# Performance work log

Hardware: AMD Instinct MI355X
Metric: run time of the kernel (lower is better)

Reference implementation:

```python
import jax, jax.numpy as jnp
import numpy as np

B, S, DM = 4, 2048, 1024
H, D, R = 16, 64, 8

def setup_inputs() -> dict:
    key = jax.random.key(0)
    ks = jax.random.split(key, 32)
    def rn(k, shape, scale=0.02):
        return jax.random.normal(k, shape, dtype=jnp.float32) * scale
    inp = {
        'queries': jax.random.normal(ks[0], (B, S, DM), dtype=jnp.float32),
        'keys':    jax.random.normal(ks[1], (B, S, DM), dtype=jnp.float32),
        'values':  jax.random.normal(ks[2], (B, S, DM), dtype=jnp.float32),
        # base projections, stored [in, out]
        'Wq_w': rn(ks[3], (DM, H * D)), 'Wq_b': jnp.zeros((H * D,), jnp.float32),
        'Wk_w': rn(ks[4], (DM, H * D)), 'Wk_b': jnp.zeros((H * D,), jnp.float32),
        'Wv_w': rn(ks[5], (DM, H * D)), 'Wv_b': jnp.zeros((H * D,), jnp.float32),
        # LoRA adapters (A: in->rank, B: rank->out), Linear layers so both have biases
        'Aq_w': rn(ks[6], (DM, R)), 'Aq_b': jnp.zeros((R,), jnp.float32),
        'Bq_w': rn(ks[7], (R, H * D)), 'Bq_b': jnp.zeros((H * D,), jnp.float32),
        'Ak_w': rn(ks[8], (DM, R)), 'Ak_b': jnp.zeros((R,), jnp.float32),
        'Bk_w': rn(ks[9], (R, H * D)), 'Bk_b': jnp.zeros((H * D,), jnp.float32),
        'Av_w': rn(ks[10], (DM, R)), 'Av_b': jnp.zeros((R,), jnp.float32),
        'Bv_w': rn(ks[11], (R, H * D)), 'Bv_b': jnp.zeros((H * D,), jnp.float32),
        # output merge
        'Wo_w': rn(ks[12], (H * D, DM)), 'Wo_b': jnp.zeros((DM,), jnp.float32),
    }
    return inp


def _attn(queries, keys, values, Wq_w, Wq_b, Wk_w, Wk_b, Wv_w, Wv_b,
          Aq_w, Aq_b, Bq_w, Bq_b, Ak_w, Ak_b, Bk_w, Bk_b, Av_w, Av_b, Bv_w, Bv_b,
          Wo_w, Wo_b):
    b, s, _ = queries.shape
    # QKV projections fused with LoRA low-rank additions
    q = queries @ Wq_w + Wq_b + ((queries @ Aq_w + Aq_b) @ Bq_w + Bq_b)
    k = keys    @ Wk_w + Wk_b + ((keys    @ Ak_w + Ak_b) @ Bk_w + Bk_b)
    # NOTE: source applies the V LoRA adapter to `keys` (self.Av(keys)) - replicated
    v = values  @ Wv_w + Wv_b + ((keys    @ Av_w + Av_b) @ Bv_w + Bv_b)
    q = q.reshape(b, s, H, D).transpose(0, 2, 1, 3)  # [B,H,S,D]
    k = k.reshape(b, s, H, D).transpose(0, 2, 1, 3)
    v = v.reshape(b, s, H, D).transpose(0, 2, 1, 3)
    att = jnp.einsum('bhqd,bhkd->bhqk', q, k)        # [B,H,Sq,Sk]
    causal = jnp.tril(jnp.ones((s, s), dtype=bool))
    att = jnp.where(causal, att, -jnp.inf)
    # NOTE: source softmaxes over dim=2 (query axis) and scales AFTER softmax
    att = jax.nn.softmax(att, axis=2) / jnp.sqrt(jnp.asarray(D, att.dtype))
    out = jnp.einsum('bhqk,bhkd->bhqd', att, v)      # [B,H,S,D]
    out = out.transpose(0, 2, 1, 3).reshape(b, s, H * D)
    return out @ Wo_w + Wo_b


def reference(queries, keys, values, Wq_w, Wq_b, Wk_w, Wk_b, Wv_w, Wv_b,
              Aq_w, Aq_b, Bq_w, Bq_b, Ak_w, Ak_b, Bk_w, Bk_b, Av_w, Av_b, Bv_w, Bv_b,
              Wo_w, Wo_b):
    return _attn(queries, keys, values, Wq_w, Wq_b, Wk_w, Wk_b, Wv_w, Wv_b,
                 Aq_w, Aq_b, Bq_w, Bq_b, Ak_w, Ak_b, Bk_w, Bk_b, Av_w, Av_b, Bv_w, Bv_b,
                 Wo_w, Wo_b)
```

## Files before the change

### kernel.cpp

```cpp
#include <hip/hip_runtime.h>
#include <math.h>
#include <stdint.h>

typedef __bf16 bf16;
typedef __bf16 bf16x8 __attribute__((ext_vector_type(8)));
typedef __bf16 bf16x4 __attribute__((ext_vector_type(4)));
typedef float  floatx4 __attribute__((ext_vector_type(4)));

#define MFMA16(a, b, c) __builtin_amdgcn_mfma_f32_16x16x32_bf16(a, b, c, 0, 0, 0)
#define EXP2(x) __builtin_amdgcn_exp2f(x)

static constexpr int S  = 2048;
static constexpr int DM = 1024;
static constexpr int Dh = 64;
static constexpr size_t QBSZ = (size_t)64 * 2048 * 64;
#define NEGBIG (-1e30f)
#define LOG2E  1.44269504088896340736f

__device__ __forceinline__ void gload16(const void* g, void* l) {
  __builtin_amdgcn_global_load_lds(
      (const __attribute__((address_space(1))) void*)(uintptr_t)g,
      (__attribute__((address_space(3))) void*)(uintptr_t)l,
      16, 0, 0);
}

__device__ __forceinline__ int swz(int row, int g) {
  return row * 64 + ((g ^ (row & 7)) << 3);
}

__global__ __launch_bounds__(256) void prep_convert(
    const float* __restrict__ q, const float* __restrict__ k,
    const float* __restrict__ v, bf16* __restrict__ X)
{
  int s = blockIdx.x;
  int c = threadIdx.x * 4;
  size_t src = (size_t)s * DM + c;
  float4 qv = *(const float4*)(q + src);
  float4 vv = *(const float4*)(v + src);
  float4 kv = *(const float4*)(k + src);
  size_t dst = (size_t)s * (3 * DM);
  bf16x4 t;
  t[0] = (bf16)qv.x; t[1] = (bf16)qv.y; t[2] = (bf16)qv.z; t[3] = (bf16)qv.w;
  *(bf16x4*)(X + dst + c) = t;
  t[0] = (bf16)vv.x; t[1] = (bf16)vv.y; t[2] = (bf16)vv.z; t[3] = (bf16)vv.w;
  *(bf16x4*)(X + dst + DM + c) = t;
  t[0] = (bf16)kv.x; t[1] = (bf16)kv.y; t[2] = (bf16)kv.z; t[3] = (bf16)kv.w;
  *(bf16x4*)(X + dst + 2 * DM + c) = t;
}

__global__ __launch_bounds__(256) void fold_weights(
    const float* __restrict__ Wq, const float* __restrict__ Aq, const float* __restrict__ Bq,
    const float* __restrict__ Wk, const float* __restrict__ Ak, const float* __restrict__ Bk,
    const float* __restrict__ Wv, const float* __restrict__ Av, const float* __restrict__ Bv,
    const float* __restrict__ Wo,
    bf16* __restrict__ WqT, bf16* __restrict__ WkT,
    bf16* __restrict__ WvT, bf16* __restrict__ WoT)
{
  __shared__ float tile[32][33];
  const int tx = threadIdx.x, ty = threadIdx.y;
  const int n0 = blockIdx.x * 32, k0 = blockIdx.y * 32;
  for (int mi = 0; mi < 5; ++mi) {
    #pragma unroll
    for (int i = 0; i < 4; ++i) {
      int k = k0 + ty + i * 8, n = n0 + tx;
      float val = 0.f;
      if (mi == 0) {
        val = Wq[(size_t)k * DM + n];
        #pragma unroll
        for (int r = 0; r < 8; ++r) val += Aq[k * 8 + r] * Bq[(size_t)r * DM + n];
        val *= LOG2E;
      } else if (mi == 1) {
        val = Wk[(size_t)k * DM + n];
        #pragma unroll
        for (int r = 0; r < 8; ++r) val += Ak[k * 8 + r] * Bk[(size_t)r * DM + n];
      } else if (mi == 2) {
        val = Wv[(size_t)k * DM + n];
      } else if (mi == 3) {
        #pragma unroll
        for (int r = 0; r < 8; ++r) val += Av[k * 8 + r] * Bv[(size_t)r * DM + n];
      } else {
        val = Wo[(size_t)k * DM + n];
      }
      tile[ty + i * 8][tx] = val;
    }
    __syncthreads();
    #pragma unroll
    for (int i = 0; i < 4; ++i) {
      int n = n0 + ty + i * 8, k = k0 + tx;
      float val = tile[tx][ty + i * 8];
      if (mi == 0)      WqT[(size_t)n * DM + k] = (bf16)val;
      else if (mi == 1) WkT[(size_t)n * DM + k] = (bf16)val;
      else if (mi == 2) WvT[(size_t)n * 2048 + k] = (bf16)val;
      else if (mi == 3) WvT[(size_t)n * 2048 + 1024 + k] = (bf16)val;
      else              WoT[(size_t)n * DM + k] = (bf16)val;
    }
    __syncthreads();
  }
}

__global__ __launch_bounds__(256) void fold_bias(
    const float* __restrict__ Wqb, const float* __restrict__ Aqb,
    const float* __restrict__ BqW, const float* __restrict__ Bqb,
    const float* __restrict__ Wkb, const float* __restrict__ Akb,
    const float* __restrict__ BkW, const float* __restrict__ Bkb,
    const float* __restrict__ Wvb, const float* __restrict__ Avb,
    const float* __restrict__ BvW, const float* __restrict__ Bvb,
    const float* __restrict__ Wob,
    float* __restrict__ bq, float* __restrict__ bk,
    float* __restrict__ bv, float* __restrict__ bo)
{
  int n = blockIdx.x * 256 + threadIdx.x;
  float aq = Wqb[n] + Bqb[n];
  float ak = Wkb[n] + Bkb[n];
  float av = Wvb[n] + Bvb[n];
  #pragma unroll
  for (int r = 0; r < 8; ++r) {
    aq += Aqb[r] * BqW[(size_t)r * DM + n];
    ak += Akb[r] * BkW[(size_t)r * DM + n];
    av += Avb[r] * BvW[(size_t)r * DM + n];
  }
  bq[n] = aq * LOG2E;
  bk[n] = ak; bv[n] = av; bo[n] = Wob[n];
}

__global__ __launch_bounds__(256) void gemm_bf16(
    const bf16* __restrict__ A, int lda,
    const bf16* __restrict__ BT, int ldb,
    const float* __restrict__ bias,
    int M, int N, int K, float oscale,
    float* __restrict__ outF, bf16* __restrict__ outB, int mode)
{
  __shared__ bf16 sA[3][128 * 32];
  __shared__ bf16 sB[3][128 * 32];
  const int tid = threadIdx.x;
  const int bm0 = blockIdx.y * 128, bn0 = blockIdx.x * 128;
  const int w = tid >> 6, lane = tid & 63, lrow = lane & 15, quad = lane >> 4;
  const int wm = (w >> 1) * 64, wn = (w & 1) * 64;

  const bf16* Abase = (mode == 1) ? (A + (size_t)(bn0 >> 10) * 2048) : A;

  const int r0 = tid >> 2;
  const int c0 = (tid & 3) ^ ((r0 >> 1) & 3);
  const bf16* Ag0 = Abase + (size_t)(bm0 + r0) * lda + c0 * 8;
  const bf16* Ag1 = Abase + (size_t)(bm0 + r0 + 64) * lda + c0 * 8;
  const bf16* Bg0 = BT + (size_t)(bn0 + r0) * ldb + c0 * 8;
  const bf16* Bg1 = BT + (size_t)(bn0 + r0 + 64) * ldb + c0 * 8;
  const int wb0 = w * 512;
  const int wb1 = 2048 + w * 512;

  int aoff[4], boff[4];
  #pragma unroll
  for (int i = 0; i < 4; ++i) {
    int ra = wm + i * 16 + lrow;
    aoff[i] = ra * 32 + ((quad ^ ((ra >> 1) & 3)) << 3);
    int rb = wn + i * 16 + lrow;
    boff[i] = rb * 32 + ((quad ^ ((rb >> 1) & 3)) << 3);
  }

  floatx4 zero = {0.f, 0.f, 0.f, 0.f};
  floatx4 acc[4][4];
  #pragma unroll
  for (int i = 0; i < 4; ++i)
    #pragma unroll
    for (int j = 0; j < 4; ++j) acc[i][j] = zero;

  auto stage = [&](int slot, int t) {
    const size_t ko = (size_t)t * 32;
    gload16(Ag0 + ko, &sA[slot][wb0]);
    gload16(Ag1 + ko, &sA[slot][wb1]);
    gload16(Bg0 + ko, &sB[slot][wb0]);
    gload16(Bg1 + ko, &sB[slot][wb1]);
  };

  const int nk = K >> 5;
  stage(0, 0);
  stage(1, 1);

  int cur = 0;
  for (int t = 0; t < nk; ++t) {
    if (t + 1 < nk) {
      asm volatile("s_waitcnt vmcnt(4)" ::: "memory");
    } else {
      asm volatile("s_waitcnt vmcnt(0)" ::: "memory");
    }
    __builtin_amdgcn_s_barrier();
    if (t + 2 < nk) {
      int nxt = cur + 2; if (nxt >= 3) nxt -= 3;
      stage(nxt, t + 2);
    }
    bf16x8 aF[4], bF[4];
    #pragma unroll
    for (int i = 0; i < 4; ++i) aF[i] = *(const bf16x8*)&sA[cur][aoff[i]];
    #pragma unroll
    for (int j = 0; j < 4; ++j) bF[j] = *(const bf16x8*)&sB[cur][boff[j]];
    #pragma unroll
    for (int i = 0; i < 4; ++i)
      #pragma unroll
      for (int j = 0; j < 4; ++j)
        acc[i][j] = MFMA16(aF[i], bF[j], acc[i][j]);
    cur = (cur == 2) ? 0 : cur + 1;
  }

  if (mode == 3) {
    #pragma unroll
    for (int i = 0; i < 4; ++i) {
      #pragma unroll
      for (int r = 0; r < 4; ++r) {
        int gm = bm0 + wm + i * 16 + quad * 4 + r;
        float bvr = bias[gm];
        int h = gm >> 6, d = gm & 63;
        #pragma unroll
        for (int j = 0; j < 4; ++j) {
          int gn = bn0 + wn + j * 16 + lrow;
          int b = gn >> 11, s = gn & 2047;
          outB[((size_t)(b * 16 + h) * 64 + d) * 2048 + s] =
              (bf16)(acc[i][j][r] + bvr);
        }
      }
    }
    return;
  }

  float bvs[4];
  #pragma unroll
  for (int j = 0; j < 4; ++j) bvs[j] = bias[bn0 + wn + j * 16 + lrow];

  #pragma unroll
  for (int i = 0; i < 4; ++i) {
    #pragma unroll
    for (int j = 0; j < 4; ++j) {
      #pragma unroll
      for (int r = 0; r < 4; ++r) {
        int gm = bm0 + wm + i * 16 + quad * 4 + r;
        int gn = bn0 + wn + j * 16 + lrow;
        float v = (acc[i][j][r] + bvs[j]) * oscale;
        if (mode == 0) {
          outF[(size_t)gm * N + gn] = v;
        } else {
          int b = gm >> 11, s = gm & 2047;
          int part = gn >> 10, h = (gn >> 6) & 15, d = gn & 63;
          outB[(size_t)part * QBSZ +
               ((size_t)(b * 16 + h) * 2048 + s) * 64 + d] = (bf16)v;
        }
      }
    }
  }
}

__global__ __launch_bounds__(256) void attn_pass1(
    const bf16* __restrict__ Qb, const bf16* __restrict__ Kb,
    float* __restrict__ statC)
{
  const int bh = blockIdx.y;
  const int x = blockIdx.x;
  const int q0a = x * 64, q0b = (31 - x) * 64;
  const int tid = threadIdx.x;
  const int w = tid >> 6, lane = tid & 63, lrow = lane & 15, quad = lane >> 4;
  const bf16* Qh = Qb + (size_t)bh * S * Dh;
  const bf16* Kh = Kb + (size_t)bh * S * Dh;

  int cbase[8];
  #pragma unroll
  for (int cf = 0; cf < 8; ++cf)
    cbase[cf] = (cf < 4) ? (q0a + cf * 16) : (q0b + (cf - 4) * 16);

  bf16x8 kf[8][2];
  #pragma unroll
  for (int cf = 0; cf < 8; ++cf) {
    const bf16* kp = Kh + (size_t)(cbase[cf] + lrow) * Dh + quad * 8;
    kf[cf][0] = *(const bf16x8*)kp;
    kf[cf][1] = *(const bf16x8*)(kp + 32);
  }

  float rs[8];
  #pragma unroll
  for (int cf = 0; cf < 8; ++cf) rs[cf] = 0.f;

  const int qs = q0a + w * 16;
  const bf16* qp0 = Qh + (size_t)(qs + lrow) * Dh + quad * 8;
  bf16x8 a0 = *(const bf16x8*)qp0, a1 = *(const bf16x8*)(qp0 + 32);

  for (int q0 = qs; q0 < S; q0 += 64) {
    bf16x8 n0 = a0, n1 = a1;
    if (q0 + 64 < S) {
      const bf16* np = Qh + (size_t)(q0 + 64 + lrow) * Dh + quad * 8;
      n0 = *(const bf16x8*)np; n1 = *(const bf16x8*)(np + 32);
    }
    #pragma unroll
    for (int cf = 0; cf < 8; ++cf) {
      const int c0f = cbase[cf];
      if (c0f > q0 + 15) continue;
      floatx4 sacc = {0.f, 0.f, 0.f, 0.f};
      sacc = MFMA16(a0, kf[cf][0], sacc);
      sacc = MFMA16(a1, kf[cf][1], sacc);
      float e0 = EXP2(sacc[0]), e1 = EXP2(sacc[1]);
      float e2 = EXP2(sacc[2]), e3 = EXP2(sacc[3]);
      if (q0 < c0f + 15) {
        int c = c0f + lrow, qb = q0 + quad * 4;
        e0 = (qb + 0 >= c) ? e0 : 0.f;
        e1 = (qb + 1 >= c) ? e1 : 0.f;
        e2 = (qb + 2 >= c) ? e2 : 0.f;
        e3 = (qb + 3 >= c) ? e3 : 0.f;
      }
      rs[cf] += (e0 + e1) + (e2 + e3);
    }
    a0 = n0; a1 = n1;
  }

  #pragma unroll
  for (int cf = 0; cf < 8; ++cf) {
    rs[cf] += __shfl_xor(rs[cf], 16, 64);
    rs[cf] += __shfl_xor(rs[cf], 32, 64);
  }

  __shared__ float sms[4][128];
  if (quad == 0) {
    #pragma unroll
    for (int cf = 0; cf < 8; ++cf)
      sms[w][cf * 16 + lrow] = rs[cf];
  }
  __syncthreads();
  if (tid < 128) {
    float sum = (sms[0][tid] + sms[1][tid]) + (sms[2][tid] + sms[3][tid]);
    int col = (tid < 64) ? (q0a + tid) : (q0b + tid - 64);
    statC[(size_t)bh * S + col] = 3.0f + __log2f(sum);
  }
}

__global__ __launch_bounds__(256) void attn_pass2(
    const bf16* __restrict__ Qb, const bf16* __restrict__ Kb,
    const bf16* __restrict__ Vt, const float* __restrict__ statC,
    bf16* __restrict__ AttOut)
{
  const int bh = blockIdx.y;
  const int x = blockIdx.x;
  const int q0a = x * 64, q0b = (31 - x) * 64;
  const int tid = threadIdx.x;
  const int w = tid >> 6, lane = tid & 63, lrow = lane & 15, quad = lane >> 4;
  const bf16* Qh = Qb + (size_t)bh * S * Dh;
  const bf16* Kh = Kb + (size_t)bh * S * Dh;
  const bf16* Vh = Vt + (size_t)bh * Dh * S;
  const float* sth = statC + (size_t)bh * S;

  __shared__ bf16 sK[64 * 64];
  __shared__ bf16 sV[64 * 64];
  __shared__ bf16 pbuf[4][32 * 64];

  const int r0m[2] = { q0a + w * 16, q0b + w * 16 };
  bf16x8 qf[2][2];
  #pragma unroll
  for (int mi = 0; mi < 2; ++mi) {
    const bf16* qp = Qh + (size_t)(r0m[mi] + lrow) * Dh + quad * 8;
    qf[mi][0] = *(const bf16x8*)qp;
    qf[mi][1] = *(const bf16x8*)(qp + 32);
  }

  floatx4 zero = {0.f, 0.f, 0.f, 0.f};
  floatx4 accO[2][4];
  #pragma unroll
  for (int mi = 0; mi < 2; ++mi)
    #pragma unroll
    for (int nf = 0; nf < 4; ++nf) accO[mi][nf] = zero;

  const int sr = tid >> 3;
  const int g  = tid & 7;
  const int nT = 32 - x;
  bf16* const pw = &pbuf[w][0];

  bf16x8 kg0 = *(const bf16x8*)(Kh + (size_t)sr * Dh + g * 8);
  bf16x8 kg1 = *(const bf16x8*)(Kh + (size_t)(sr + 32) * Dh + g * 8);
  bf16x8 vg0 = *(const bf16x8*)(Vh + (size_t)sr * S + g * 8);
  bf16x8 vg1 = *(const bf16x8*)(Vh + (size_t)(sr + 32) * S + g * 8);

  for (int kt = 0; kt < nT; ++kt) {
    const int kc = kt * 64;
    __syncthreads();
    *(bf16x8*)&sK[swz(sr, g)]      = kg0;
    *(bf16x8*)&sK[swz(sr + 32, g)] = kg1;
    *(bf16x8*)&sV[swz(sr, g)]      = vg0;
    *(bf16x8*)&sV[swz(sr + 32, g)] = vg1;
    float4 c4[4];
    #pragma unroll
    for (int cf = 0; cf < 4; ++cf)
      c4[cf] = *(const float4*)&sth[kc + cf * 16 + quad * 4];
    __syncthreads();
    if (kt + 1 < nT) {
      const int kn = kc + 64;
      kg0 = *(const bf16x8*)(Kh + (size_t)(kn + sr) * Dh + g * 8);
      kg1 = *(const bf16x8*)(Kh + (size_t)(kn + sr + 32) * Dh + g * 8);
      vg0 = *(const bf16x8*)(Vh + (size_t)sr * S + kn + g * 8);
      vg1 = *(const bf16x8*)(Vh + (size_t)(sr + 32) * S + kn + g * 8);
    }

    bool actH[2][2];
    #pragma unroll
    for (int mi = 0; mi < 2; ++mi) {
      actH[mi][0] = kc      <= r0m[mi] + 15;
      actH[mi][1] = kc + 32 <= r0m[mi] + 15;
    }

    #pragma unroll
    for (int cf = 0; cf < 4; ++cf) {
      const int hh = cf >> 1;
      if (!actH[0][hh] && !actH[1][hh]) continue;
      const int c0f = kc + cf * 16;
      const int cl = cf * 16;
      bf16x8 kf0 = *(const bf16x8*)&sK[swz(cl + lrow, quad)];
      bf16x8 kf1 = *(const bf16x8*)&sK[swz(cl + lrow, 4 + quad)];
      const float* cc = &c4[cf].x;
      const int crb = c0f + quad * 4;
      #pragma unroll
      for (int mi = 0; mi < 2; ++mi) {
        if (!actH[mi][hh]) continue;
        const int r0 = r0m[mi];
        const int gq = cf * 2 + (quad >> 1);
        const int poff = (mi * 16 + lrow) * 64 +
                         ((gq ^ (lrow & 7)) << 3) + (quad & 1) * 4;
        bf16x4 pk;
        if (c0f > r0 + 15) {
          pk[0] = pk[1] = pk[2] = pk[3] = (bf16)0.f;
        } else {
          floatx4 sacc = zero;
          sacc = MFMA16(kf0, qf[mi][0], sacc);
          sacc = MFMA16(kf1, qf[mi][1], sacc);
          const bool fullf = (c0f + 15 <= r0);
          const int qlane = r0 + lrow;
          #pragma unroll
          for (int r = 0; r < 4; ++r) {
            float p = EXP2(sacc[r] - cc[r]);
            if (!fullf) p = (crb + r <= qlane) ? p : 0.f;
            pk[r] = (bf16)p;
          }
        }
        *(bf16x4*)(pw + poff) = pk;
      }
    }

    #pragma unroll
    for (int hh = 0; hh < 2; ++hh) {
      if (!actH[0][hh] && !actH[1][hh]) continue;
      bf16x8 vf[4];
      #pragma unroll
      for (int nf = 0; nf < 4; ++nf)
        vf[nf] = *(const bf16x8*)&sV[swz(nf * 16 + lrow, hh * 4 + quad)];
      #pragma unroll
      for (int mi = 0; mi < 2; ++mi) {
        if (!actH[mi][hh]) continue;
        bf16x8 pf = *(const bf16x8*)(pw + swz(mi * 16 + lrow, hh * 4 + quad));
        #pragma unroll
        for (int nf = 0; nf < 4; ++nf)
          accO[mi][nf] = MFMA16(pf, vf[nf], accO[mi][nf]);
      }
    }
  }

  const int b = bh >> 4, h = bh & 15;
  #pragma unroll
  for (int mi = 0; mi < 2; ++mi) {
    #pragma unroll
    for (int nf = 0; nf < 4; ++nf) {
      #pragma unroll
      for (int r = 0; r < 4; ++r) {
        int qq = r0m[mi] + quad * 4 + r;
        int d = nf * 16 + lrow;
        AttOut[((size_t)(b * S + qq)) * DM + h * 64 + d] = (bf16)accO[mi][nf][r];
      }
    }
  }
}

extern "C" void kernel_launch(void* const* d_in, const int* in_sizes, int n_in,
                              void* d_out, int out_size, void* d_ws, size_t ws_size,
                              hipStream_t stream) {
  (void)in_sizes; (void)n_in; (void)out_size; (void)ws_size;
  const float* queries = (const float*)d_in[0];
  const float* keys    = (const float*)d_in[1];
  const float* values  = (const float*)d_in[2];
  const float* Wq_w = (const float*)d_in[3];  const float* Wq_b = (const float*)d_in[4];
  const float* Wk_w = (const float*)d_in[5];  const float* Wk_b = (const float*)d_in[6];
  const float* Wv_w = (const float*)d_in[7];  const float* Wv_b = (const float*)d_in[8];
  const float* Aq_w = (const float*)d_in[9];  const float* Aq_b = (const float*)d_in[10];
  const float* Bq_w = (const float*)d_in[11]; const float* Bq_b = (const float*)d_in[12];
  const float* Ak_w = (const float*)d_in[13]; const float* Ak_b = (const float*)d_in[14];
  const float* Bk_w = (const float*)d_in[15]; const float* Bk_b = (const float*)d_in[16];
  const float* Av_w = (const float*)d_in[17]; const float* Av_b = (const float*)d_in[18];
  const float* Bv_w = (const float*)d_in[19]; const float* Bv_b = (const float*)d_in[20];
  const float* Wo_w = (const float*)d_in[21]; const float* Wo_b = (const float*)d_in[22];
  float* out = (float*)d_out;

  char* ws = (char*)d_ws;
  size_t off = 0;
  auto alloc = [&](size_t bytes) -> void* {
    void* p = ws + off;
    off += (bytes + 255) & ~(size_t)255;
    return p;
  };
  bf16*  X_all  = (bf16*)alloc((size_t)8192 * 3072 * 2);
  bf16*  Qb     = (bf16*)alloc(QBSZ * 2 * 2);
  bf16*  Kb     = Qb + QBSZ;
  bf16*  Vt     = (bf16*)alloc((size_t)64 * 64 * 2048 * 2);
  bf16*  AttOut = (bf16*)alloc((size_t)8192 * 1024 * 2);
  bf16*  WqkT   = (bf16*)alloc((size_t)2048 * 1024 * 2);
  bf16*  WvT    = (bf16*)alloc((size_t)1024 * 2048 * 2);
  bf16*  WoT    = (bf16*)alloc((size_t)1024 * 1024 * 2);
  float* bqk    = (float*)alloc(2048 * 4);
  float* bv     = (float*)alloc(1024 * 4);
  float* bo     = (float*)alloc(1024 * 4);
  float* statC  = (float*)alloc((size_t)64 * 2048 * 4);

  prep_convert<<<8192, 256, 0, stream>>>(queries, keys, values, X_all);
  fold_weights<<<dim3(32, 32), dim3(32, 8), 0, stream>>>(
      Wq_w, Aq_w, Bq_w, Wk_w, Ak_w, Bk_w, Wv_w, Av_w, Bv_w, Wo_w,
      WqkT, WqkT + (size_t)1024 * 1024, WvT, WoT);
  fold_bias<<<4, 256, 0, stream>>>(
      Wq_b, Aq_b, Bq_w, Bq_b, Wk_b, Ak_b, Bk_w, Bk_b,
      Wv_b, Av_b, Bv_w, Bv_b, Wo_b, bqk, bqk + 1024, bv, bo);

  gemm_bf16<<<dim3(16, 64), 256, 0, stream>>>(X_all, 3072, WqkT, 1024, bqk, 8192, 2048, 1024, 1.0f, nullptr, Qb, 1);
  gemm_bf16<<<dim3(64, 8), 256, 0, stream>>>(WvT, 2048, X_all + 1024, 3072, bv, 1024, 8192, 2048, 1.0f, nullptr, Vt, 3);

  attn_pass1<<<dim3(16, 64), 256, 0, stream>>>(Qb, Kb, statC);
  attn_pass2<<<dim3(16, 64), 256, 0, stream>>>(Qb, Kb, Vt, statC, AttOut);

  gemm_bf16<<<dim3(8, 64), 256, 0, stream>>>(AttOut, 1024, WoT, 1024, bo, 8192, 1024, 1024, 1.0f, out, nullptr, 0);
}
```

Before: 425.0 us.

## Merge QK and V projection GEMMs into one launch with double buffering

Measured after the change: 423.8 us. Within noise of the previous version (-0.3%).

```diff
diff --git a/kernel.cpp b/kernel.cpp
--- a/kernel.cpp
+++ b/kernel.cpp
@@ -123,6 +123,132 @@
   bk[n] = ak; bv[n] = av; bo[n] = Wob[n];
 }
 
+__global__ __launch_bounds__(256, 4) void gemm_qkv(
+    const bf16* __restrict__ X, const bf16* __restrict__ WqkT,
+    const bf16* __restrict__ WvT,
+    const float* __restrict__ bqk, const float* __restrict__ bv,
+    bf16* __restrict__ Qb, bf16* __restrict__ Vt)
+{
+  __shared__ bf16 sA[2][128 * 32];
+  __shared__ bf16 sB[2][128 * 32];
+  const int tid = threadIdx.x;
+  const int w = tid >> 6, lane = tid & 63, lrow = lane & 15, quad = lane >> 4;
+  const int wm = (w >> 1) * 64, wn = (w & 1) * 64;
+
+  int id = blockIdx.x;
+  const bf16 *A, *BT;
+  const float* bias;
+  bf16* outB;
+  int lda, ldb, K, bm0, bn0, mode;
+  if (id < 1024) {
+    int bx = id & 15, by = id >> 4;
+    bm0 = by * 128; bn0 = bx * 128;
+    A = X + (size_t)(bn0 >> 10) * 2048;
+    lda = 3072; BT = WqkT; ldb = 1024; K = 1024;
+    bias = bqk; outB = Qb; mode = 1;
+  } else {
+    id -= 1024;
+    int bx = id & 63, by = id >> 6;
+    bm0 = by * 128; bn0 = bx * 128;
+    A = WvT; lda = 2048;
+    BT = X + 1024; ldb = 3072; K = 2048;
+    bias = bv; outB = Vt; mode = 3;
+  }
+
+  const int r0 = tid >> 2;
+  const int c0 = (tid & 3) ^ ((r0 >> 1) & 3);
+  const bf16* Ag0 = A  + (size_t)(bm0 + r0) * lda + c0 * 8;
+  const bf16* Ag1 = A  + (size_t)(bm0 + r0 + 64) * lda + c0 * 8;
+  const bf16* Bg0 = BT + (size_t)(bn0 + r0) * ldb + c0 * 8;
+  const bf16* Bg1 = BT + (size_t)(bn0 + r0 + 64) * ldb + c0 * 8;
+  const int wb0 = w * 512;
+  const int wb1 = 2048 + w * 512;
+
+  int aoff[4], boff[4];
+  #pragma unroll
+  for (int i = 0; i < 4; ++i) {
+    int ra = wm + i * 16 + lrow;
+    aoff[i] = ra * 32 + ((quad ^ ((ra >> 1) & 3)) << 3);
+    int rb = wn + i * 16 + lrow;
+    boff[i] = rb * 32 + ((quad ^ ((rb >> 1) & 3)) << 3);
+  }
+
+  floatx4 zero = {0.f, 0.f, 0.f, 0.f};
+  floatx4 acc[4][4];
+  #pragma unroll
+  for (int i = 0; i < 4; ++i)
+    #pragma unroll
+    for (int j = 0; j < 4; ++j) acc[i][j] = zero;
+
+  auto stage = [&](int slot, int t) {
+    const size_t ko = (size_t)t * 32;
+    gload16(Ag0 + ko, &sA[slot][wb0]);
+    gload16(Ag1 + ko, &sA[slot][wb1]);
+    gload16(Bg0 + ko, &sB[slot][wb0]);
+    gload16(Bg1 + ko, &sB[slot][wb1]);
+  };
+
+  const int nk = K >> 5;
+  stage(0, 0);
+
+  for (int t = 0; t < nk; ++t) {
+    const int cur = t & 1;
+    __syncthreads();
+    if (t + 1 < nk) stage(cur ^ 1, t + 1);
+    bf16x8 aF[4], bF[4];
+    #pragma unroll
+    for (int i = 0; i < 4; ++i) aF[i] = *(const bf16x8*)&sA[cur][aoff[i]];
+    #pragma unroll
+    for (int j = 0; j < 4; ++j) bF[j] = *(const bf16x8*)&sB[cur][boff[j]];
+    #pragma unroll
+    for (int i = 0; i < 4; ++i)
+      #pragma unroll
+      for (int j = 0; j < 4; ++j)
+        acc[i][j] = MFMA16(aF[i], bF[j], acc[i][j]);
+  }
+
+  if (mode == 3) {
+    #pragma unroll
+    for (int i = 0; i < 4; ++i) {
+      #pragma unroll
+      for (int r = 0; r < 4; ++r) {
+        int gm = bm0 + wm + i * 16 + quad * 4 + r;
+        float bvr = bias[gm];
+        int h = gm >> 6, d = gm & 63;
+        #pragma unroll
+        for (int j = 0; j < 4; ++j) {
+          int gn = bn0 + wn + j * 16 + lrow;
+          int b = gn >> 11, s = gn & 2047;
+          outB[((size_t)(b * 16 + h) * 64 + d) * 2048 + s] =
+              (bf16)(acc[i][j][r] + bvr);
+        }
+      }
+    }
+    return;
+  }
+
+  float bvs[4];
+  #pragma unroll
+  for (int j = 0; j < 4; ++j) bvs[j] = bias[bn0 + wn + j * 16 + lrow];
+
+  #pragma unroll
+  for (int i = 0; i < 4; ++i) {
+    #pragma unroll
+    for (int j = 0; j < 4; ++j) {
+      #pragma unroll
+      for (int r = 0; r < 4; ++r) {
+        int gm = bm0 + wm + i * 16 + quad * 4 + r;
+        int gn = bn0 + wn + j * 16 + lrow;
+        float v = acc[i][j][r] + bvs[j];
+        int b = gm >> 11, s = gm & 2047;
+        int part = gn >> 10, h = (gn >> 6) & 15, d = gn & 63;
+        outB[(size_t)part * QBSZ +
+             ((size_t)(b * 16 + h) * 2048 + s) * 64 + d] = (bf16)v;
+      }
+    }
+  }
+}
+
 __global__ __launch_bounds__(256) void gemm_bf16(
     const bf16* __restrict__ A, int lda,
     const bf16* __restrict__ BT, int ldb,
@@ -137,12 +263,10 @@
   const int w = tid >> 6, lane = tid & 63, lrow = lane & 15, quad = lane >> 4;
   const int wm = (w >> 1) * 64, wn = (w & 1) * 64;
 
-  const bf16* Abase = (mode == 1) ? (A + (size_t)(bn0 >> 10) * 2048) : A;
-
   const int r0 = tid >> 2;
   const int c0 = (tid & 3) ^ ((r0 >> 1) & 3);
-  const bf16* Ag0 = Abase + (size_t)(bm0 + r0) * lda + c0 * 8;
-  const bf16* Ag1 = Abase + (size_t)(bm0 + r0 + 64) * lda + c0 * 8;
+  const bf16* Ag0 = A + (size_t)(bm0 + r0) * lda + c0 * 8;
+  const bf16* Ag1 = A + (size_t)(bm0 + r0 + 64) * lda + c0 * 8;
   const bf16* Bg0 = BT + (size_t)(bn0 + r0) * ldb + c0 * 8;
   const bf16* Bg1 = BT + (size_t)(bn0 + r0 + 64) * ldb + c0 * 8;
   const int wb0 = w * 512;
@@ -201,26 +325,6 @@
     cur = (cur == 2) ? 0 : cur + 1;
   }
 
-  if (mode == 3) {
-    #pragma unroll
-    for (int i = 0; i < 4; ++i) {
-      #pragma unroll
-      for (int r = 0; r < 4; ++r) {
-        int gm = bm0 + wm + i * 16 + quad * 4 + r;
-        float bvr = bias[gm];
-        int h = gm >> 6, d = gm & 63;
-        #pragma unroll
-        for (int j = 0; j < 4; ++j) {
-          int gn = bn0 + wn + j * 16 + lrow;
-          int b = gn >> 11, s = gn & 2047;
-          outB[((size_t)(b * 16 + h) * 64 + d) * 2048 + s] =
-              (bf16)(acc[i][j][r] + bvr);
-        }
-      }
-    }
-    return;
-  }
-
   float bvs[4];
   #pragma unroll
   for (int j = 0; j < 4; ++j) bvs[j] = bias[bn0 + wn + j * 16 + lrow];
@@ -233,15 +337,7 @@
       for (int r = 0; r < 4; ++r) {
         int gm = bm0 + wm + i * 16 + quad * 4 + r;
         int gn = bn0 + wn + j * 16 + lrow;
-        float v = (acc[i][j][r] + bvs[j]) * oscale;
-        if (mode == 0) {
-          outF[(size_t)gm * N + gn] = v;
-        } else {
-          int b = gm >> 11, s = gm & 2047;
-          int part = gn >> 10, h = (gn >> 6) & 15, d = gn & 63;
-          outB[(size_t)part * QBSZ +
-               ((size_t)(b * 16 + h) * 2048 + s) * 64 + d] = (bf16)v;
-        }
+        outF[(size_t)gm * N + gn] = (acc[i][j][r] + bvs[j]) * oscale;
       }
     }
   }
@@ -516,8 +612,7 @@
       Wq_b, Aq_b, Bq_w, Bq_b, Wk_b, Ak_b, Bk_w, Bk_b,
       Wv_b, Av_b, Bv_w, Bv_b, Wo_b, bqk, bqk + 1024, bv, bo);
 
-  gemm_bf16<<<dim3(16, 64), 256, 0, stream>>>(X_all, 3072, WqkT, 1024, bqk, 8192, 2048, 1024, 1.0f, nullptr, Qb, 1);
-  gemm_bf16<<<dim3(64, 8), 256, 0, stream>>>(WvT, 2048, X_all + 1024, 3072, bv, 1024, 8192, 2048, 1.0f, nullptr, Vt, 3);
+  gemm_qkv<<<1536, 256, 0, stream>>>(X_all, WqkT, WvT, bqk, bv, Qb, Vt);
 
   attn_pass1<<<dim3(16, 64), 256, 0, stream>>>(Qb, Kb, statC);
   attn_pass2<<<dim3(16, 64), 256, 0, stream>>>(Qb, Kb, Vt, statC, AttOut);
```
